# Kernel tuning notes

Measured on AMD Instinct MI355X. Metric: run time of the kernel, lower is better.

## Reference

```python
import jax, jax.numpy as jnp
import numpy as np

NUM_NODES = 200000
B = 65536          # n_id batch size
E = 131072         # events per direction
D_MEM = 128
D_RAW = 128
D_TIME = 128
T_MAX = 1000000


def setup_inputs() -> dict:
    key = jax.random.key(0)
    ks = jax.random.split(key, 16)
    inp = {
        'memory': jax.random.normal(ks[0], (NUM_NODES, D_MEM), jnp.float32),
        'last_update': jax.random.randint(ks[1], (NUM_NODES,), 0, 1000, jnp.int64),
        'n_id': jnp.arange(B, dtype=jnp.int64),
        'src_s': jax.random.randint(ks[2], (E,), 0, B, jnp.int64),
        'dst_s': jax.random.randint(ks[3], (E,), 0, B, jnp.int64),
        't_s': jax.random.randint(ks[4], (E,), 0, T_MAX, jnp.int64),
        'raw_msg_s': jax.random.normal(ks[5], (E, D_RAW), jnp.float32),
        'src_d': jax.random.randint(ks[6], (E,), 0, B, jnp.int64),
        'dst_d': jax.random.randint(ks[7], (E,), 0, B, jnp.int64),
        't_d': jax.random.randint(ks[8], (E,), 0, T_MAX, jnp.int64),
        'raw_msg_d': jax.random.normal(ks[9], (E, D_RAW), jnp.float32),
        'w_time': jax.random.normal(ks[10], (D_TIME, 1), jnp.float32) * 0.1,
        'b_time': jax.random.normal(ks[11], (D_TIME,), jnp.float32) * 0.1,
        'W_ih': jax.random.normal(ks[12], (3 * D_MEM, 2 * D_MEM + D_RAW + D_TIME), jnp.float32) * 0.05,
        'W_hh': jax.random.normal(ks[13], (3 * D_MEM, D_MEM), jnp.float32) * 0.05,
        'b_ih': jax.random.normal(ks[14], (3 * D_MEM,), jnp.float32) * 0.05,
        'b_hh': jax.random.normal(ks[15], (3 * D_MEM,), jnp.float32) * 0.05,
    }
    return inp


def _time_enc(t_rel, w_time, b_time):
    # Linear(1, time_dim) followed by cos: cos(t * w + b)
    return jnp.cos(t_rel.astype(jnp.float32)[:, None] * w_time[:, 0][None, :] + b_time)


def reference(memory, last_update, n_id, src_s, dst_s, t_s, raw_msg_s,
              src_d, dst_d, t_d, raw_msg_d, w_time, b_time, W_ih, W_hh, b_ih, b_hh):
    nb = n_id.shape[0]
    # assoc: global node id -> local index within n_id
    assoc = jnp.zeros((memory.shape[0],), dtype=jnp.int32).at[n_id].set(
        jnp.arange(nb, dtype=jnp.int32))

    # source-side messages (IdentityMessage = concat)
    t_enc_s = _time_enc(t_s - last_update[src_s], w_time, b_time)
    msg_s = jnp.concatenate([memory[src_s], memory[dst_s], raw_msg_s, t_enc_s], axis=-1)

    # destination-side messages
    t_enc_d = _time_enc(t_d - last_update[dst_d], w_time, b_time)
    msg_d = jnp.concatenate([memory[dst_d], memory[src_d], raw_msg_d, t_enc_d], axis=-1)

    idx = jnp.concatenate([src_s, dst_d], axis=0)       # [2E] global ids
    msg = jnp.concatenate([msg_s, msg_d], axis=0)       # [2E, 512]
    t = jnp.concatenate([t_s, t_d], axis=0)             # [2E]
    loc = assoc[idx]                                     # [2E] local ids

    # LastAggregator: per local node, pick the message with max t (ties -> latest position)
    ne = t.shape[0]
    key = t * ne + jnp.arange(ne, dtype=t.dtype)         # encode (t, position)
    maxkey = jax.ops.segment_max(key, loc, num_segments=nb)
    count = jax.ops.segment_sum(jnp.ones_like(loc), loc, num_segments=nb)
    has = count > 0
    argm = jnp.where(has, maxkey % ne, 0)
    aggr = jnp.where(has[:, None], msg[argm], 0.0)       # [nb, 512]

    # GRUCell(x=aggr, h=memory[n_id])
    h = memory[n_id]
    gi = aggr @ W_ih.T + b_ih
    gh = h @ W_hh.T + b_hh
    gi_r, gi_z, gi_n = jnp.split(gi, 3, axis=-1)
    gh_r, gh_z, gh_n = jnp.split(gh, 3, axis=-1)
    r = jax.nn.sigmoid(gi_r + gh_r)
    z = jax.nn.sigmoid(gi_z + gh_z)
    n = jnp.tanh(gi_n + r * gh_n)
    new_memory = (1.0 - z) * n + z * h

    new_last_update = last_update.at[idx].set(t)[n_id]
    return new_memory, new_last_update
```

## Files before the change

kernel.cpp:

```cpp
#include <hip/hip_runtime.h>
#include <math.h>

#define NB        65536
#define EV        131072
#define NE        (2*EV)
#define DM        128
#define NO2       512
#define BM        64
#define NST       10
#define THREADS   512

typedef float f32x4  __attribute__((ext_vector_type(4)));
typedef float f32x16 __attribute__((ext_vector_type(16)));
typedef int   i32x4  __attribute__((ext_vector_type(4)));
typedef int   i32x8  __attribute__((ext_vector_type(8)));
typedef unsigned long long u64;

__device__ __forceinline__ float fcos_rev(float rev) {
    float r; asm("v_cos_f32 %0, %1" : "=v"(r) : "v"(rev)); return r;
}
__device__ __forceinline__ float fexp2(float x) {
    float r; asm("v_exp_f32 %0, %1" : "=v"(r) : "v"(x)); return r;
}
__device__ __forceinline__ float frcp(float x) {
    float r; asm("v_rcp_f32 %0, %1" : "=v"(r) : "v"(x)); return r;
}
__device__ __forceinline__ float fast_cos(float arg) {
    double rv = (double)arg * 0.15915494309189535;
    rv -= floor(rv);
    return fcos_rev((float)rv);
}
__device__ __forceinline__ float fsigmoid(float x) {
    x = fminf(fmaxf(x, -30.f), 30.f);
    float e = fexp2(-1.44269504088896f * x);
    return frcp(1.f + e);
}
__device__ __forceinline__ float ftanh_(float x) {
    x = fminf(fmaxf(x, -15.f), 15.f);
    float e = fexp2(-2.88539008177793f * x);
    return (1.f - e) * frcp(1.f + e);
}

#if defined(__has_builtin) && __has_builtin(__builtin_amdgcn_cvt_pk_fp8_f32)
__device__ __forceinline__ unsigned pack4_fp8(float f0, float f1, float f2, float f3) {
    int v = __builtin_amdgcn_cvt_pk_fp8_f32(f0, f1, 0, false);
    v = __builtin_amdgcn_cvt_pk_fp8_f32(f2, f3, v, true);
    return (unsigned)v;
}
#else
__device__ __forceinline__ unsigned enc1_fp8(float x) {
    unsigned u = __float_as_uint(x);
    unsigned s = (u >> 24) & 0x80u;
    float a = fabsf(x);
    if (!(a >= 0.001953125f)) return s;
    if (a > 448.f) a = 448.f;
    int e; float mf = frexpf(a, &e);
    int E = e + 6, mant;
    if (E <= 0) {
        mant = (int)(a * 512.f + 0.5f);
        if (mant > 7) return s | 0x08u;
        return s | (unsigned)mant;
    }
    mant = (int)((mf * 2.f - 1.f) * 8.f + 0.5f);
    if (mant == 8) { mant = 0; ++E; }
    if (E > 15) { E = 15; mant = 6; }
    if (E == 15 && mant == 7) mant = 6;
    return s | (unsigned)(E << 3) | (unsigned)mant;
}
__device__ __forceinline__ unsigned pack4_fp8(float f0, float f1, float f2, float f3) {
    return enc1_fp8(f0) | (enc1_fp8(f1) << 8) | (enc1_fp8(f2) << 16) | (enc1_fp8(f3) << 24);
}
#endif

__global__ void prep_k(const int* __restrict__ src_s, const int* __restrict__ t_s,
                       const int* __restrict__ dst_d, const int* __restrict__ t_d,
                       u64* __restrict__ keyarr, u64* __restrict__ lukey,
                       const float* __restrict__ W_ih, const float* __restrict__ W_hh,
                       const float* __restrict__ b_ih, const float* __restrict__ b_hh,
                       unsigned char* __restrict__ wp8, float* __restrict__ bp) {
    int bid = blockIdx.x;
    if (bid < NE / 256) {
        int e = bid * 256 + threadIdx.x;
        int g, t;
        if (e < EV) { g = src_s[e];      t = t_s[e]; }
        else        { g = dst_d[e - EV]; t = t_d[e - EV]; }
        u64 key = ((u64)(unsigned)t << 18) + (u64)(unsigned)e + 1ull;
        atomicMax(&keyarr[g], key);
        u64 lk = ((u64)(unsigned)(e + 1) << 20) | (u64)(unsigned)t;
        atomicMax(&lukey[g], lk);
        return;
    }
    int idx = (bid - NE / 256) * 256 + threadIdx.x;
    int col = idx / 80, g = idx - col * 80;
    int step = g >> 3, sl = g & 7;
    int ck = ((sl >> 1) ^ ((col >> 1) & 3));
    int k0 = step * 64 + ck * 16 + (sl & 1) * 8;
    int d = col >> 2, gate = col & 3;
    float f[8];
    #pragma unroll
    for (int j = 0; j < 8; ++j) {
        int c = k0 + j;
        float v = 0.f;
        if (c < 512) {
            int row = (gate == 0) ? d : (gate == 1) ? 128 + d : (gate == 2) ? 256 + d : -1;
            if (row >= 0) v = W_ih[(size_t)row * 512 + c];
        } else {
            int ch = c - 512;
            int row = (gate == 0) ? d : (gate == 1) ? 128 + d : (gate == 3) ? 256 + d : -1;
            if (row >= 0) v = W_hh[(size_t)row * 128 + ch];
        }
        f[j] = v * 16.f;
    }
    unsigned lo = pack4_fp8(f[0], f[1], f[2], f[3]);
    unsigned hi = pack4_fp8(f[4], f[5], f[6], f[7]);
    *(u64*)(wp8 + (size_t)step * 32768 + (size_t)col * 64 + (size_t)sl * 8)
        = (u64)lo | ((u64)hi << 32);
    if (g == 0) {
        float bv = (gate == 0) ? b_ih[d] + b_hh[d]
                 : (gate == 1) ? b_ih[128 + d] + b_hh[128 + d]
                 : (gate == 2) ? b_ih[256 + d] : b_hh[256 + d];
        bp[col] = bv;
    }
}

__global__ __launch_bounds__(THREADS, 4) void gemm_gru_k(
    const float* __restrict__ memory, const int* __restrict__ last_update,
    const int* __restrict__ src_s, const int* __restrict__ dst_s,
    const int* __restrict__ t_s, const float* __restrict__ raw_s,
    const int* __restrict__ src_d, const int* __restrict__ dst_d,
    const int* __restrict__ t_d, const float* __restrict__ raw_d,
    const float* __restrict__ w_time, const float* __restrict__ b_time,
    const unsigned char* __restrict__ wp8, const float* __restrict__ bp,
    const u64* __restrict__ keyarr, const u64* __restrict__ lukey,
    float* __restrict__ out_mem, float* __restrict__ out_lu)
{
    __shared__ __align__(16) char smem[74752];
    unsigned char* sA = (unsigned char*)smem;
    unsigned char* sB = (unsigned char*)(smem + 8192);
    float* sW = (float*)(smem + 73728);
    float* sBt= (float*)(smem + 74240);

    const int tid = threadIdx.x;
    const int m0  = blockIdx.x * BM;
    const int ln  = tid & 63, wn = tid >> 6;
    const int lg  = ln >> 5;

    if (tid < DM) { sW[tid] = w_time[tid]; sBt[tid] = b_time[tid]; }

    const int ar = tid >> 3, ac = tid & 7;
    const int m  = m0 + ar;
    const u64 kk = keyarr[m];
    const int rv = (kk != 0ull);
    int a_ = 0, b_ = 0, t_ = 0;
    const float* pR = raw_s;
    if (kk) {
        int e = (int)((kk - 1ull) & (u64)(NE - 1));
        if (e < EV) { a_ = src_s[e]; b_ = dst_s[e]; t_ = t_s[e]; pR = raw_s + (size_t)e * DM; }
        else { int e2 = e - EV; a_ = dst_d[e2]; b_ = src_d[e2]; t_ = t_d[e2]; pR = raw_d + (size_t)e2 * DM; }
    }
    const float rt = rv ? (float)(t_ - last_update[a_]) : 0.f;
    const float* pA = memory + (size_t)a_ * DM;
    const float* pB = memory + (size_t)b_ * DM;
    const float* pH = memory + (size_t)m  * DM;

    float4 pv0, pv1;
    auto PREF_A = [&](int step) {
        int seg = step >> 1;
        if (seg == 3) return;
        const float* base = (seg == 0) ? pA : (seg == 1) ? pB : (seg == 2) ? pR : pH;
        int off = ((step & 1) << 6) + (ac << 3);
        pv0 = *(const float4*)(base + off);
        pv1 = *(const float4*)(base + off + 4);
    };
    auto STAGE_B = [&](int step, int buf) {
        const unsigned char* src = wp8 + (size_t)step * 32768 + (size_t)tid * 16;
        unsigned char* dst = sB + (size_t)buf * 32768 + (size_t)tid * 16;
        #pragma unroll
        for (int i = 0; i < 4; ++i)
            __builtin_amdgcn_global_load_lds(
                (const __attribute__((address_space(1))) void*)(src + i * 8192),
                (__attribute__((address_space(3))) void*)(dst + i * 8192), 16, 0, 0);
    };
    auto WRITE_A = [&](int step, int buf) {
        int seg = step >> 1;
        float f0, f1, f2, f3, f4, f5, f6, f7;
        if (seg == 3) {
            int coff = ((step & 1) << 6) + (ac << 3);
            f0 = fast_cos(__fadd_rn(__fmul_rn(rt, sW[coff+0]), sBt[coff+0]));
            f1 = fast_cos(__fadd_rn(__fmul_rn(rt, sW[coff+1]), sBt[coff+1]));
            f2 = fast_cos(__fadd_rn(__fmul_rn(rt, sW[coff+2]), sBt[coff+2]));
            f3 = fast_cos(__fadd_rn(__fmul_rn(rt, sW[coff+3]), sBt[coff+3]));
            f4 = fast_cos(__fadd_rn(__fmul_rn(rt, sW[coff+4]), sBt[coff+4]));
            f5 = fast_cos(__fadd_rn(__fmul_rn(rt, sW[coff+5]), sBt[coff+5]));
            f6 = fast_cos(__fadd_rn(__fmul_rn(rt, sW[coff+6]), sBt[coff+6]));
            f7 = fast_cos(__fadd_rn(__fmul_rn(rt, sW[coff+7]), sBt[coff+7]));
        } else {
            f0 = pv0.x; f1 = pv0.y; f2 = pv0.z; f3 = pv0.w;
            f4 = pv1.x; f5 = pv1.y; f6 = pv1.z; f7 = pv1.w;
        }
        if (seg < 4 && !rv) { f0=f1=f2=f3=f4=f5=f6=f7 = 0.f; }
        unsigned lo = pack4_fp8(f0, f1, f2, f3);
        unsigned hi = pack4_fp8(f4, f5, f6, f7);
        u64 q = (u64)lo | ((u64)hi << 32);
        *(u64*)(sA + buf * 4096 + ar * 64
                + (((ac >> 1) ^ ((ar >> 1) & 3)) << 4) + ((ac & 1) << 3)) = q;
    };

    f32x16 acc[2][2];
    #pragma unroll
    for (int mf = 0; mf < 2; ++mf)
        #pragma unroll
        for (int nf = 0; nf < 2; ++nf)
            #pragma unroll
            for (int j = 0; j < 16; ++j) acc[mf][nf][j] = 0.f;

    PREF_A(0);
    WRITE_A(0, 0);
    STAGE_B(0, 0);
    PREF_A(1);
    asm volatile("s_waitcnt vmcnt(2) lgkmcnt(0)" ::: "memory");
    __builtin_amdgcn_sched_barrier(0);
    __builtin_amdgcn_s_barrier();

    #pragma unroll
    for (int k = 0; k < NST; ++k) {
        const int cur = k & 1, nxt = cur ^ 1;

        if (k < NST - 1) {
            WRITE_A(k + 1, nxt);
            __builtin_amdgcn_sched_barrier(0);
            STAGE_B(k + 1, nxt);
            __builtin_amdgcn_sched_barrier(0);
        }

        i32x8 af[2], bf[2];
        #pragma unroll
        for (int mf = 0; mf < 2; ++mf) {
            int r = mf * 32 + (ln & 31), sw = (r >> 1) & 3;
            i32x4 q0 = *(const i32x4*)(sA + cur * 4096 + r * 64 + (((2*lg+0) ^ sw) << 4));
            i32x4 q1 = *(const i32x4*)(sA + cur * 4096 + r * 64 + (((2*lg+1) ^ sw) << 4));
            af[mf] = (i32x8){q0.x,q0.y,q0.z,q0.w, q1.x,q1.y,q1.z,q1.w};
        }
        #pragma unroll
        for (int nf = 0; nf < 2; ++nf) {
            int c = wn * 64 + nf * 32 + (ln & 31), sw = (c >> 1) & 3;
            i32x4 q0 = *(const i32x4*)(sB + cur * 32768 + c * 64 + (((2*lg+0) ^ sw) << 4));
            i32x4 q1 = *(const i32x4*)(sB + cur * 32768 + c * 64 + (((2*lg+1) ^ sw) << 4));
            bf[nf] = (i32x8){q0.x,q0.y,q0.z,q0.w, q1.x,q1.y,q1.z,q1.w};
        }
        __builtin_amdgcn_sched_barrier(0);

        const bool pf = (k + 2 <= NST - 1) && (((k + 2) >> 1) != 3);
        if (pf) PREF_A(k + 2);
        __builtin_amdgcn_sched_barrier(0);

        __builtin_amdgcn_s_setprio(1);
        #pragma unroll
        for (int mf = 0; mf < 2; ++mf)
            #pragma unroll
            for (int nf = 0; nf < 2; ++nf)
                acc[mf][nf] = __builtin_amdgcn_mfma_scale_f32_32x32x64_f8f6f4(
                    af[mf], bf[nf], acc[mf][nf], 0, 0, 0, 127, 0, 127);
        __builtin_amdgcn_s_setprio(0);

        if (k < NST - 1) {
            __builtin_amdgcn_sched_barrier(0);
            if (pf) asm volatile("s_waitcnt vmcnt(2) lgkmcnt(0)" ::: "memory");
            else    asm volatile("s_waitcnt vmcnt(0) lgkmcnt(0)" ::: "memory");
            __builtin_amdgcn_sched_barrier(0);
            __builtin_amdgcn_s_barrier();
        }
    }

    if (tid < BM) {
        u64 lk = lukey[m0 + tid];
        out_lu[m0 + tid] = lk ? (float)(unsigned)(lk & 0xFFFFFull)
                              : (float)last_update[m0 + tid];
    }
    __syncthreads();

    float* ep = (float*)(smem + wn * 8704);
    const int erow = ln >> 1, half = ln & 1;
    const int d0 = wn * 16 + half * 8;
    const float ds = 0.0625f;

    #pragma unroll
    for (int mf = 0; mf < 2; ++mf) {
        #pragma unroll
        for (int nf = 0; nf < 2; ++nf)
            #pragma unroll
            for (int reg = 0; reg < 16; ++reg) {
                int r32 = (reg & 3) + 8 * (reg >> 2) + 4 * lg;
                ep[r32 * 68 + nf * 32 + (ln & 31)] = acc[mf][nf][reg] * ds;
            }
        asm volatile("s_waitcnt lgkmcnt(0)" ::: "memory");

        const int gm = m0 + mf * 32 + erow;
        const float* gr = ep + erow * 68 + half * 32;
        float res[8];
        f32x4 h0 = *(const f32x4*)(memory + (size_t)gm * DM + d0);
        f32x4 h1 = *(const f32x4*)(memory + (size_t)gm * DM + d0 + 4);
        #pragma unroll
        for (int q = 0; q < 8; ++q) {
            f32x4 g  = *(const f32x4*)(gr + q * 4);
            f32x4 bb = *(const f32x4*)(bp + (d0 + q) * 4);
            float rg = fsigmoid(g.x + bb.x);
            float zg = fsigmoid(g.y + bb.y);
            float ng = ftanh_(g.z + bb.z + rg * (g.w + bb.w));
            float hh = (q < 4) ? ((const float*)&h0)[q] : ((const float*)&h1)[q - 4];
            res[q] = (1.f - zg) * ng + zg * hh;
        }
        *(f32x4*)(out_mem + (size_t)gm * DM + d0)     = *(const f32x4*)res;
        *(f32x4*)(out_mem + (size_t)gm * DM + d0 + 4) = *(const f32x4*)(res + 4);
        if (mf == 0) asm volatile("s_waitcnt lgkmcnt(0)" ::: "memory");
    }
}

extern "C" void kernel_launch(void* const* d_in, const int* in_sizes, int n_in,
                              void* d_out, int out_size, void* d_ws, size_t ws_size,
                              hipStream_t stream) {
    const float* memory      = (const float*)d_in[0];
    const int*   last_update = (const int*)d_in[1];
    const int*   src_s       = (const int*)d_in[3];
    const int*   dst_s       = (const int*)d_in[4];
    const int*   t_s         = (const int*)d_in[5];
    const float* raw_s       = (const float*)d_in[6];
    const int*   src_d       = (const int*)d_in[7];
    const int*   dst_d       = (const int*)d_in[8];
    const int*   t_d         = (const int*)d_in[9];
    const float* raw_d       = (const float*)d_in[10];
    const float* w_time      = (const float*)d_in[11];
    const float* b_time      = (const float*)d_in[12];
    const float* W_ih        = (const float*)d_in[13];
    const float* W_hh        = (const float*)d_in[14];
    const float* b_ih        = (const float*)d_in[15];
    const float* b_hh        = (const float*)d_in[16];

    char* ws = (char*)d_ws;
    u64* keyarr = (u64*)ws;
    u64* lukey  = (u64*)(ws + 524288);
    unsigned char* wp8 = (unsigned char*)(ws + 1048576);
    float* bp = (float*)(ws + 1376256);

    hipMemsetAsync(d_ws, 0, 1048576, stream);

    prep_k<<<NE / 256 + (NO2 * 80) / 256, 256, 0, stream>>>(
        src_s, t_s, dst_d, t_d, keyarr, lukey, W_ih, W_hh, b_ih, b_hh, wp8, bp);

    float* out_mem = (float*)d_out;
    float* out_lu  = out_mem + (size_t)NB * DM;
    gemm_gru_k<<<NB / BM, THREADS, 0, stream>>>(memory, last_update,
        src_s, dst_s, t_s, raw_s, src_d, dst_d, t_d, raw_d,
        w_time, b_time, wp8, bp, keyarr, lukey, out_mem, out_lu);
}
```

Before: 78.63 us.

## Enlarge GEMM tile to 128 rows with triple-buffered 16x16x32 FP8 MFMA pipeline

Doubles the row tile per block from 64 to 128 and splits the 8 waves into a 2x4 grid, each computing a 64x128 output sub-tile with 16x16x32 FP8 MFMAs in place of the scaled 32x32x64 instruction. A/B staging moves from double to triple buffering with a two-step lookahead, and the weight packing layout in prep changes to match. The goal is more reuse of each weight tile per block and better overlap of loads with MFMA work, at the cost of more LDS per block (occupancy cut to 2 blocks per CU), more barriers per step, and scalar instead of vector stores in the epilogue.

```diff
diff --git a/kernel.cpp b/kernel.cpp
--- a/kernel.cpp
+++ b/kernel.cpp
@@ -1,19 +1,16 @@
 #include <hip/hip_runtime.h>
 #include <math.h>
 
-#define NB        65536
-#define EV        131072
-#define NE        (2*EV)
-#define DM        128
-#define NO2       512
-#define BM        64
-#define NST       10
-#define THREADS   512
-
-typedef float f32x4  __attribute__((ext_vector_type(4)));
-typedef float f32x16 __attribute__((ext_vector_type(16)));
-typedef int   i32x4  __attribute__((ext_vector_type(4)));
-typedef int   i32x8  __attribute__((ext_vector_type(8)));
+#define NB 65536
+#define EV 131072
+#define NE (2*EV)
+#define DM 128
+#define BM 128
+#define NT 10
+#define THREADS 512
+
+typedef float f32x4 __attribute__((ext_vector_type(4)));
+typedef int   i32x4 __attribute__((ext_vector_type(4)));
 typedef unsigned long long u64;
 
 __device__ __forceinline__ float fcos_rev(float rev) {
@@ -91,10 +88,10 @@
         return;
     }
     int idx = (bid - NE / 256) * 256 + threadIdx.x;
-    int col = idx / 80, g = idx - col * 80;
-    int step = g >> 3, sl = g & 7;
-    int ck = ((sl >> 1) ^ ((col >> 1) & 3));
-    int k0 = step * 64 + ck * 16 + (sl & 1) * 8;
+    int t = idx >> 12, r = idx & 4095;
+    int col = r >> 3, slot = r & 7;
+    int g = slot ^ ((col >> 1) & 3);
+    int k0 = t * 64 + g * 8;
     int d = col >> 2, gate = col & 3;
     float f[8];
     #pragma unroll
@@ -113,9 +110,8 @@
     }
     unsigned lo = pack4_fp8(f[0], f[1], f[2], f[3]);
     unsigned hi = pack4_fp8(f[4], f[5], f[6], f[7]);
-    *(u64*)(wp8 + (size_t)step * 32768 + (size_t)col * 64 + (size_t)sl * 8)
-        = (u64)lo | ((u64)hi << 32);
-    if (g == 0) {
+    *(u64*)(wp8 + (size_t)idx * 8) = (u64)lo | ((u64)hi << 32);
+    if (k0 == 0) {
         float bv = (gate == 0) ? b_ih[d] + b_hh[d]
                  : (gate == 1) ? b_ih[128 + d] + b_hh[128 + d]
                  : (gate == 2) ? b_ih[256 + d] : b_hh[256 + d];
@@ -123,7 +119,7 @@
     }
 }
 
-__global__ __launch_bounds__(THREADS, 4) void gemm_gru_k(
+__global__ __launch_bounds__(THREADS, 2) void gemm_gru_k(
     const float* __restrict__ memory, const int* __restrict__ last_update,
     const int* __restrict__ src_s, const int* __restrict__ dst_s,
     const int* __restrict__ t_s, const float* __restrict__ raw_s,
@@ -134,20 +130,21 @@
     const u64* __restrict__ keyarr, const u64* __restrict__ lukey,
     float* __restrict__ out_mem, float* __restrict__ out_lu)
 {
-    __shared__ __align__(16) char smem[74752];
+    __shared__ __align__(16) char smem[123904];
     unsigned char* sA = (unsigned char*)smem;
-    unsigned char* sB = (unsigned char*)(smem + 8192);
-    float* sW = (float*)(smem + 73728);
-    float* sBt= (float*)(smem + 74240);
+    unsigned char* sB = (unsigned char*)(smem + 24576);
+    float* sW  = (float*)(smem + 122880);
+    float* sBt = (float*)(smem + 123392);
 
     const int tid = threadIdx.x;
     const int m0  = blockIdx.x * BM;
-    const int ln  = tid & 63, wn = tid >> 6;
-    const int lg  = ln >> 5;
+    const int ln  = tid & 63, wid = tid >> 6;
+    const int wr  = wid >> 2, wc = wid & 3;
+    const int l2  = ln >> 4, rl = ln & 15;
 
     if (tid < DM) { sW[tid] = w_time[tid]; sBt[tid] = b_time[tid]; }
 
-    const int ar = tid >> 3, ac = tid & 7;
+    const int ar = tid >> 2, kc = tid & 3;
     const int m  = m0 + ar;
     const u64 kk = keyarr[m];
     const int rv = (kk != 0ull);
@@ -163,112 +160,132 @@
     const float* pB = memory + (size_t)b_ * DM;
     const float* pH = memory + (size_t)m  * DM;
 
-    float4 pv0, pv1;
-    auto PREF_A = [&](int step) {
-        int seg = step >> 1;
-        if (seg == 3) return;
-        const float* base = (seg == 0) ? pA : (seg == 1) ? pB : (seg == 2) ? pR : pH;
-        int off = ((step & 1) << 6) + (ac << 3);
-        pv0 = *(const float4*)(base + off);
-        pv1 = *(const float4*)(base + off + 4);
+    float4 pv[4];
+    auto PREF_A = [&](int t) {
+        const float* base; int off;
+        if (t < 2)      { base = pA; off = (t & 1) * 64; }
+        else if (t < 4) { base = pB; off = (t & 1) * 64; }
+        else if (t < 6) { base = pR; off = (t & 1) * 64; }
+        else            { base = pH; off = (t - 8) * 64; }
+        const float* p = base + off + kc * 16;
+        pv[0] = *(const float4*)(p);
+        pv[1] = *(const float4*)(p + 4);
+        pv[2] = *(const float4*)(p + 8);
+        pv[3] = *(const float4*)(p + 12);
     };
-    auto STAGE_B = [&](int step, int buf) {
-        const unsigned char* src = wp8 + (size_t)step * 32768 + (size_t)tid * 16;
-        unsigned char* dst = sB + (size_t)buf * 32768 + (size_t)tid * 16;
+    auto GLL_B = [&](int t) {
+        const unsigned char* src = wp8 + (size_t)t * 32768 + (size_t)tid * 16;
+        unsigned char* dst = sB + (size_t)(t % 3) * 32768 + (size_t)tid * 16;
         #pragma unroll
         for (int i = 0; i < 4; ++i)
             __builtin_amdgcn_global_load_lds(
                 (const __attribute__((address_space(1))) void*)(src + i * 8192),
                 (__attribute__((address_space(3))) void*)(dst + i * 8192), 16, 0, 0);
     };
-    auto WRITE_A = [&](int step, int buf) {
-        int seg = step >> 1;
-        float f0, f1, f2, f3, f4, f5, f6, f7;
-        if (seg == 3) {
-            int coff = ((step & 1) << 6) + (ac << 3);
-            f0 = fast_cos(__fadd_rn(__fmul_rn(rt, sW[coff+0]), sBt[coff+0]));
-            f1 = fast_cos(__fadd_rn(__fmul_rn(rt, sW[coff+1]), sBt[coff+1]));
-            f2 = fast_cos(__fadd_rn(__fmul_rn(rt, sW[coff+2]), sBt[coff+2]));
-            f3 = fast_cos(__fadd_rn(__fmul_rn(rt, sW[coff+3]), sBt[coff+3]));
-            f4 = fast_cos(__fadd_rn(__fmul_rn(rt, sW[coff+4]), sBt[coff+4]));
-            f5 = fast_cos(__fadd_rn(__fmul_rn(rt, sW[coff+5]), sBt[coff+5]));
-            f6 = fast_cos(__fadd_rn(__fmul_rn(rt, sW[coff+6]), sBt[coff+6]));
-            f7 = fast_cos(__fadd_rn(__fmul_rn(rt, sW[coff+7]), sBt[coff+7]));
+    auto WRITE_A = [&](int t) {
+        unsigned p0, p1, p2, p3;
+        if (t >= 6 && t < 8) {
+            int coff = (t & 1) * 64 + kc * 16;
+            float c[16];
+            #pragma unroll
+            for (int j = 0; j < 16; ++j)
+                c[j] = fast_cos(__fadd_rn(__fmul_rn(rt, sW[coff + j]), sBt[coff + j]));
+            p0 = pack4_fp8(c[0], c[1], c[2], c[3]);
+            p1 = pack4_fp8(c[4], c[5], c[6], c[7]);
+            p2 = pack4_fp8(c[8], c[9], c[10], c[11]);
+            p3 = pack4_fp8(c[12], c[13], c[14], c[15]);
         } else {
-            f0 = pv0.x; f1 = pv0.y; f2 = pv0.z; f3 = pv0.w;
-            f4 = pv1.x; f5 = pv1.y; f6 = pv1.z; f7 = pv1.w;
+            p0 = pack4_fp8(pv[0].x, pv[0].y, pv[0].z, pv[0].w);
+            p1 = pack4_fp8(pv[1].x, pv[1].y, pv[1].z, pv[1].w);
+            p2 = pack4_fp8(pv[2].x, pv[2].y, pv[2].z, pv[2].w);
+            p3 = pack4_fp8(pv[3].x, pv[3].y, pv[3].z, pv[3].w);
         }
-        if (seg < 4 && !rv) { f0=f1=f2=f3=f4=f5=f6=f7 = 0.f; }
-        unsigned lo = pack4_fp8(f0, f1, f2, f3);
-        unsigned hi = pack4_fp8(f4, f5, f6, f7);
-        u64 q = (u64)lo | ((u64)hi << 32);
-        *(u64*)(sA + buf * 4096 + ar * 64
-                + (((ac >> 1) ^ ((ar >> 1) & 3)) << 4) + ((ac & 1) << 3)) = q;
+        if (t < 8 && !rv) { p0 = p1 = p2 = p3 = 0u; }
+        int swz = (ar >> 1) & 3;
+        i32x4 v = (swz & 1) ? (i32x4){(int)p2, (int)p3, (int)p0, (int)p1}
+                            : (i32x4){(int)p0, (int)p1, (int)p2, (int)p3};
+        *(i32x4*)(sA + (size_t)(t % 3) * 8192 + ar * 64 + (((2 * kc) ^ (swz & 2)) << 3)) = v;
     };
 
-    f32x16 acc[2][2];
+    f32x4 acc[4][8];
     #pragma unroll
-    for (int mf = 0; mf < 2; ++mf)
-        #pragma unroll
-        for (int nf = 0; nf < 2; ++nf)
-            #pragma unroll
-            for (int j = 0; j < 16; ++j) acc[mf][nf][j] = 0.f;
+    for (int mf = 0; mf < 4; ++mf)
+        #pragma unroll
+        for (int nf = 0; nf < 8; ++nf)
+            acc[mf][nf] = (f32x4){0.f, 0.f, 0.f, 0.f};
 
     PREF_A(0);
-    WRITE_A(0, 0);
-    STAGE_B(0, 0);
+    WRITE_A(0);
     PREF_A(1);
-    asm volatile("s_waitcnt vmcnt(2) lgkmcnt(0)" ::: "memory");
+    WRITE_A(1);
+    GLL_B(0);
+    GLL_B(1);
+    PREF_A(2);
+    asm volatile("s_waitcnt vmcnt(8) lgkmcnt(0)" ::: "memory");
     __builtin_amdgcn_sched_barrier(0);
     __builtin_amdgcn_s_barrier();
 
     #pragma unroll
-    for (int k = 0; k < NST; ++k) {
-        const int cur = k & 1, nxt = cur ^ 1;
-
-        if (k < NST - 1) {
-            WRITE_A(k + 1, nxt);
-            __builtin_amdgcn_sched_barrier(0);
-            STAGE_B(k + 1, nxt);
-            __builtin_amdgcn_sched_barrier(0);
-        }
-
-        i32x8 af[2], bf[2];
-        #pragma unroll
-        for (int mf = 0; mf < 2; ++mf) {
-            int r = mf * 32 + (ln & 31), sw = (r >> 1) & 3;
-            i32x4 q0 = *(const i32x4*)(sA + cur * 4096 + r * 64 + (((2*lg+0) ^ sw) << 4));
-            i32x4 q1 = *(const i32x4*)(sA + cur * 4096 + r * 64 + (((2*lg+1) ^ sw) << 4));
-            af[mf] = (i32x8){q0.x,q0.y,q0.z,q0.w, q1.x,q1.y,q1.z,q1.w};
-        }
-        #pragma unroll
-        for (int nf = 0; nf < 2; ++nf) {
-            int c = wn * 64 + nf * 32 + (ln & 31), sw = (c >> 1) & 3;
-            i32x4 q0 = *(const i32x4*)(sB + cur * 32768 + c * 64 + (((2*lg+0) ^ sw) << 4));
-            i32x4 q1 = *(const i32x4*)(sB + cur * 32768 + c * 64 + (((2*lg+1) ^ sw) << 4));
-            bf[nf] = (i32x8){q0.x,q0.y,q0.z,q0.w, q1.x,q1.y,q1.z,q1.w};
-        }
-        __builtin_amdgcn_sched_barrier(0);
-
-        const bool pf = (k + 2 <= NST - 1) && (((k + 2) >> 1) != 3);
-        if (pf) PREF_A(k + 2);
-        __builtin_amdgcn_sched_barrier(0);
-
-        __builtin_amdgcn_s_setprio(1);
-        #pragma unroll
-        for (int mf = 0; mf < 2; ++mf)
-            #pragma unroll
-            for (int nf = 0; nf < 2; ++nf)
-                acc[mf][nf] = __builtin_amdgcn_mfma_scale_f32_32x32x64_f8f6f4(
-                    af[mf], bf[nf], acc[mf][nf], 0, 0, 0, 127, 0, 127);
-        __builtin_amdgcn_s_setprio(0);
-
-        if (k < NST - 1) {
-            __builtin_amdgcn_sched_barrier(0);
-            if (pf) asm volatile("s_waitcnt vmcnt(2) lgkmcnt(0)" ::: "memory");
-            else    asm volatile("s_waitcnt vmcnt(0) lgkmcnt(0)" ::: "memory");
+    for (int t = 0; t < NT; ++t) {
+        #pragma unroll
+        for (int ph = 0; ph < 4; ++ph) {
+            const int mh = ph >> 1, nh = ph & 1;
+
+            long afr[2][2], bfr[4][2];
+            {
+                const unsigned char* aB = sA + (size_t)(t % 3) * 8192;
+                #pragma unroll
+                for (int mi = 0; mi < 2; ++mi) {
+                    int r = wr * 64 + (mh * 2 + mi) * 16 + rl;
+                    int so = ((l2 ^ ((r >> 1) & 3)) << 3);
+                    afr[mi][0] = *(const long*)(aB + r * 64 + so);
+                    afr[mi][1] = *(const long*)(aB + r * 64 + so + 32);
+                }
+                const unsigned char* bB = sB + (size_t)(t % 3) * 32768;
+                #pragma unroll
+                for (int ni = 0; ni < 4; ++ni) {
+                    int c = wc * 128 + (nh * 4 + ni) * 16 + rl;
+                    int so = ((l2 ^ ((c >> 1) & 3)) << 3);
+                    bfr[ni][0] = *(const long*)(bB + c * 64 + so);
+                    bfr[ni][1] = *(const long*)(bB + c * 64 + so + 32);
+                }
+            }
+            if (ph == 0 && t + 2 < NT) { WRITE_A(t + 2); GLL_B(t + 2); }
+            if (ph == 1 && t + 3 < NT && !(t + 3 == 6 || t + 3 == 7)) PREF_A(t + 3);
+
             __builtin_amdgcn_sched_barrier(0);
             __builtin_amdgcn_s_barrier();
+            asm volatile("s_waitcnt lgkmcnt(0)" ::: "memory");
+            __builtin_amdgcn_sched_barrier(0);
+
+            __builtin_amdgcn_s_setprio(1);
+            #pragma unroll
+            for (int ks = 0; ks < 2; ++ks)
+                #pragma unroll
+                for (int mi = 0; mi < 2; ++mi)
+                    #pragma unroll
+                    for (int ni = 0; ni < 4; ++ni)
+                        acc[mh * 2 + mi][nh * 4 + ni] =
+                            __builtin_amdgcn_mfma_f32_16x16x32_fp8_fp8(
+                                afr[mi][ks], bfr[ni][ks],
+                                acc[mh * 2 + mi][nh * 4 + ni], 0, 0, 0);
+            __builtin_amdgcn_s_setprio(0);
+            __builtin_amdgcn_sched_barrier(0);
+
+            if (ph == 3) {
+                if (t < NT - 1) {
+                    if (t == 3 || t == 4 || t == 7)
+                        asm volatile("s_waitcnt vmcnt(4) lgkmcnt(0)" ::: "memory");
+                    else if (t == 8)
+                        asm volatile("s_waitcnt vmcnt(0) lgkmcnt(0)" ::: "memory");
+                    else
+                        asm volatile("s_waitcnt vmcnt(8) lgkmcnt(0)" ::: "memory");
+                    __builtin_amdgcn_sched_barrier(0);
+                    __builtin_amdgcn_s_barrier();
+                }
+            } else {
+                __builtin_amdgcn_s_barrier();
+            }
         }
     }
 
@@ -279,40 +296,33 @@
     }
     __syncthreads();
 
-    float* ep = (float*)(smem + wn * 8704);
-    const int erow = ln >> 1, half = ln & 1;
-    const int d0 = wn * 16 + half * 8;
-    const float ds = 0.0625f;
+    float* ep = (float*)(smem + wid * 8448);
+    const int row16 = ln >> 2, dq = ln & 3;
+    const int d8 = wc * 32 + dq * 8;
+    const float dsc = 0.0625f;
 
     #pragma unroll
-    for (int mf = 0; mf < 2; ++mf) {
-        #pragma unroll
-        for (int nf = 0; nf < 2; ++nf)
+    for (int mf = 0; mf < 4; ++mf) {
+        #pragma unroll
+        for (int nf = 0; nf < 8; ++nf)
             #pragma unroll
-            for (int reg = 0; reg < 16; ++reg) {
-                int r32 = (reg & 3) + 8 * (reg >> 2) + 4 * lg;
-                ep[r32 * 68 + nf * 32 + (ln & 31)] = acc[mf][nf][reg] * ds;
-            }
+            for (int reg = 0; reg < 4; ++reg)
+                ep[(l2 * 4 + reg) * 132 + nf * 16 + rl] = acc[mf][nf][reg] * dsc;
         asm volatile("s_waitcnt lgkmcnt(0)" ::: "memory");
 
-        const int gm = m0 + mf * 32 + erow;
-        const float* gr = ep + erow * 68 + half * 32;
-        float res[8];
-        f32x4 h0 = *(const f32x4*)(memory + (size_t)gm * DM + d0);
-        f32x4 h1 = *(const f32x4*)(memory + (size_t)gm * DM + d0 + 4);
+        const int gm = m0 + wr * 64 + mf * 16 + row16;
         #pragma unroll
         for (int q = 0; q < 8; ++q) {
-            f32x4 g  = *(const f32x4*)(gr + q * 4);
-            f32x4 bb = *(const f32x4*)(bp + (d0 + q) * 4);
+            int q2 = (q + dq) & 7;
+            f32x4 g  = *(const f32x4*)(ep + row16 * 132 + dq * 32 + q2 * 4);
+            f32x4 bb = *(const f32x4*)(bp + (size_t)(d8 + q2) * 4);
             float rg = fsigmoid(g.x + bb.x);
             float zg = fsigmoid(g.y + bb.y);
             float ng = ftanh_(g.z + bb.z + rg * (g.w + bb.w));
-            float hh = (q < 4) ? ((const float*)&h0)[q] : ((const float*)&h1)[q - 4];
-            res[q] = (1.f - zg) * ng + zg * hh;
+            float hh = memory[(size_t)gm * DM + d8 + q2];
+            out_mem[(size_t)gm * DM + d8 + q2] = (1.f - zg) * ng + zg * hh;
         }
-        *(f32x4*)(out_mem + (size_t)gm * DM + d0)     = *(const f32x4*)res;
-        *(f32x4*)(out_mem + (size_t)gm * DM + d0 + 4) = *(const f32x4*)(res + 4);
-        if (mf == 0) asm volatile("s_waitcnt lgkmcnt(0)" ::: "memory");
+        if (mf < 3) asm volatile("s_waitcnt lgkmcnt(0)" ::: "memory");
     }
 }
 
@@ -344,7 +354,7 @@
 
     hipMemsetAsync(d_ws, 0, 1048576, stream);
 
-    prep_k<<<NE / 256 + (NO2 * 80) / 256, 256, 0, stream>>>(
+    prep_k<<<NE / 256 + 160, 256, 0, stream>>>(
         src_s, t_s, dst_d, t_d, keyarr, lukey, W_ih, W_hh, b_ih, b_hh, wp8, bp);
 
     float* out_mem = (float*)d_out;
```

Measured after the change: 109.6 us. 39.4% more time.

## Split activation gather and fp8 packing into a separate kernel before the GEMM

Applied to the files above, without the earlier changes.

The gather of memory rows, raw messages and the time-encoding cosines moves out of the GEMM main loop into a new build kernel. That kernel writes a pre-swizzled fp8 A matrix into the output buffer, which is reused as scratch. The GEMM kernel then streams A tiles straight into LDS with async loads, just as it does for B, and only packs the hidden-state rows itself. The weight-packing layout is rewritten to 16-byte chunks. The aim is to take irregular gathers and transcendental work off the MFMA critical path, at the cost of an extra launch and an extra global write and read of the packed A matrix.

```diff
diff --git a/kernel.cpp b/kernel.cpp
--- a/kernel.cpp
+++ b/kernel.cpp
@@ -1,14 +1,13 @@
 #include <hip/hip_runtime.h>
 #include <math.h>
 
-#define NB        65536
-#define EV        131072
-#define NE        (2*EV)
-#define DM        128
-#define NO2       512
-#define BM        64
-#define NST       10
-#define THREADS   512
+#define NB 65536
+#define EV 131072
+#define NE (2*EV)
+#define DM 128
+#define BM 64
+#define NT 10
+#define THREADS 512
 
 typedef float f32x4  __attribute__((ext_vector_type(4)));
 typedef float f32x16 __attribute__((ext_vector_type(16)));
@@ -72,85 +71,73 @@
 }
 #endif
 
-__global__ void prep_k(const int* __restrict__ src_s, const int* __restrict__ t_s,
+__global__ void scan_k(const int* __restrict__ src_s, const int* __restrict__ t_s,
                        const int* __restrict__ dst_d, const int* __restrict__ t_d,
-                       u64* __restrict__ keyarr, u64* __restrict__ lukey,
-                       const float* __restrict__ W_ih, const float* __restrict__ W_hh,
-                       const float* __restrict__ b_ih, const float* __restrict__ b_hh,
-                       unsigned char* __restrict__ wp8, float* __restrict__ bp) {
+                       u64* __restrict__ keyarr, u64* __restrict__ lukey) {
+    int e = blockIdx.x * 256 + threadIdx.x;
+    int g, t;
+    if (e < EV) { g = src_s[e];      t = t_s[e]; }
+    else        { g = dst_d[e - EV]; t = t_d[e - EV]; }
+    u64 key = ((u64)(unsigned)t << 18) + (u64)(unsigned)e + 1ull;
+    atomicMax(&keyarr[g], key);
+    u64 lk = ((u64)(unsigned)(e + 1) << 20) | (u64)(unsigned)t;
+    atomicMax(&lukey[g], lk);
+}
+
+__global__ void build_k(const u64* __restrict__ keyarr, const u64* __restrict__ lukey,
+                        const float* __restrict__ memory, const int* __restrict__ last_update,
+                        const int* __restrict__ src_s, const int* __restrict__ dst_s,
+                        const int* __restrict__ t_s, const float* __restrict__ raw_s,
+                        const int* __restrict__ src_d, const int* __restrict__ dst_d,
+                        const int* __restrict__ t_d, const float* __restrict__ raw_d,
+                        const float* __restrict__ w_time, const float* __restrict__ b_time,
+                        const float* __restrict__ W_ih, const float* __restrict__ W_hh,
+                        const float* __restrict__ b_ih, const float* __restrict__ b_hh,
+                        unsigned char* __restrict__ wp8, float* __restrict__ bp,
+                        unsigned char* __restrict__ a8, float* __restrict__ out_lu) {
     int bid = blockIdx.x;
-    if (bid < NE / 256) {
-        int e = bid * 256 + threadIdx.x;
-        int g, t;
-        if (e < EV) { g = src_s[e];      t = t_s[e]; }
-        else        { g = dst_d[e - EV]; t = t_d[e - EV]; }
-        u64 key = ((u64)(unsigned)t << 18) + (u64)(unsigned)e + 1ull;
-        atomicMax(&keyarr[g], key);
-        u64 lk = ((u64)(unsigned)(e + 1) << 20) | (u64)(unsigned)t;
-        atomicMax(&lukey[g], lk);
+    if (bid < 80) {
+        int idx = bid * 256 + threadIdx.x;
+        int t = idx >> 11, r = idx & 2047;
+        int c = r >> 2, pg = r & 3;
+        int g = pg ^ ((c >> 1) & 3);
+        int k0 = t * 64 + g * 16;
+        int d = c >> 2, gate = c & 3;
+        float f[16];
+        #pragma unroll
+        for (int j = 0; j < 16; ++j) {
+            int k = k0 + j;
+            float v = 0.f;
+            if (k < 512) {
+                int row = (gate == 0) ? d : (gate == 1) ? 128 + d : (gate == 2) ? 256 + d : -1;
+                if (row >= 0) v = W_ih[(size_t)row * 512 + k];
+            } else {
+                int ch = k - 512;
+                int row = (gate == 0) ? d : (gate == 1) ? 128 + d : (gate == 3) ? 256 + d : -1;
+                if (row >= 0) v = W_hh[(size_t)row * 128 + ch];
+            }
+            f[j] = v * 16.f;
+        }
+        i32x4 v;
+        v.x = (int)pack4_fp8(f[0], f[1], f[2], f[3]);
+        v.y = (int)pack4_fp8(f[4], f[5], f[6], f[7]);
+        v.z = (int)pack4_fp8(f[8], f[9], f[10], f[11]);
+        v.w = (int)pack4_fp8(f[12], f[13], f[14], f[15]);
+        *(i32x4*)(wp8 + (size_t)idx * 16) = v;
+        if (k0 == 0) {
+            float bv = (gate == 0) ? b_ih[d] + b_hh[d]
+                     : (gate == 1) ? b_ih[128 + d] + b_hh[128 + d]
+                     : (gate == 2) ? b_ih[256 + d] : b_hh[256 + d];
+            bp[c] = bv;
+        }
         return;
     }
-    int idx = (bid - NE / 256) * 256 + threadIdx.x;
-    int col = idx / 80, g = idx - col * 80;
-    int step = g >> 3, sl = g & 7;
-    int ck = ((sl >> 1) ^ ((col >> 1) & 3));
-    int k0 = step * 64 + ck * 16 + (sl & 1) * 8;
-    int d = col >> 2, gate = col & 3;
-    float f[8];
-    #pragma unroll
-    for (int j = 0; j < 8; ++j) {
-        int c = k0 + j;
-        float v = 0.f;
-        if (c < 512) {
-            int row = (gate == 0) ? d : (gate == 1) ? 128 + d : (gate == 2) ? 256 + d : -1;
-            if (row >= 0) v = W_ih[(size_t)row * 512 + c];
-        } else {
-            int ch = c - 512;
-            int row = (gate == 0) ? d : (gate == 1) ? 128 + d : (gate == 3) ? 256 + d : -1;
-            if (row >= 0) v = W_hh[(size_t)row * 128 + ch];
-        }
-        f[j] = v * 16.f;
-    }
-    unsigned lo = pack4_fp8(f[0], f[1], f[2], f[3]);
-    unsigned hi = pack4_fp8(f[4], f[5], f[6], f[7]);
-    *(u64*)(wp8 + (size_t)step * 32768 + (size_t)col * 64 + (size_t)sl * 8)
-        = (u64)lo | ((u64)hi << 32);
-    if (g == 0) {
-        float bv = (gate == 0) ? b_ih[d] + b_hh[d]
-                 : (gate == 1) ? b_ih[128 + d] + b_hh[128 + d]
-                 : (gate == 2) ? b_ih[256 + d] : b_hh[256 + d];
-        bp[col] = bv;
-    }
-}
-
-__global__ __launch_bounds__(THREADS, 4) void gemm_gru_k(
-    const float* __restrict__ memory, const int* __restrict__ last_update,
-    const int* __restrict__ src_s, const int* __restrict__ dst_s,
-    const int* __restrict__ t_s, const float* __restrict__ raw_s,
-    const int* __restrict__ src_d, const int* __restrict__ dst_d,
-    const int* __restrict__ t_d, const float* __restrict__ raw_d,
-    const float* __restrict__ w_time, const float* __restrict__ b_time,
-    const unsigned char* __restrict__ wp8, const float* __restrict__ bp,
-    const u64* __restrict__ keyarr, const u64* __restrict__ lukey,
-    float* __restrict__ out_mem, float* __restrict__ out_lu)
-{
-    __shared__ __align__(16) char smem[74752];
-    unsigned char* sA = (unsigned char*)smem;
-    unsigned char* sB = (unsigned char*)(smem + 8192);
-    float* sW = (float*)(smem + 73728);
-    float* sBt= (float*)(smem + 74240);
-
-    const int tid = threadIdx.x;
-    const int m0  = blockIdx.x * BM;
-    const int ln  = tid & 63, wn = tid >> 6;
-    const int lg  = ln >> 5;
-
-    if (tid < DM) { sW[tid] = w_time[tid]; sBt[tid] = b_time[tid]; }
-
-    const int ar = tid >> 3, ac = tid & 7;
-    const int m  = m0 + ar;
-    const u64 kk = keyarr[m];
-    const int rv = (kk != 0ull);
+    int blk = bid - 80;
+    int m0 = blk * 64;
+    int r = threadIdx.x >> 2, pg = threadIdx.x & 3;
+    int m = m0 + r;
+    u64 kk = keyarr[m];
+    int rv = (kk != 0ull);
     int a_ = 0, b_ = 0, t_ = 0;
     const float* pR = raw_s;
     if (kk) {
@@ -161,19 +148,80 @@
     const float rt = rv ? (float)(t_ - last_update[a_]) : 0.f;
     const float* pA = memory + (size_t)a_ * DM;
     const float* pB = memory + (size_t)b_ * DM;
-    const float* pH = memory + (size_t)m  * DM;
-
-    float4 pv0, pv1;
-    auto PREF_A = [&](int step) {
-        int seg = step >> 1;
-        if (seg == 3) return;
-        const float* base = (seg == 0) ? pA : (seg == 1) ? pB : (seg == 2) ? pR : pH;
-        int off = ((step & 1) << 6) + (ac << 3);
-        pv0 = *(const float4*)(base + off);
-        pv1 = *(const float4*)(base + off + 4);
+    if (pg == 0) {
+        u64 lk = lukey[m];
+        out_lu[m] = lk ? (float)(unsigned)(lk & 0xFFFFFull) : (float)last_update[m];
+    }
+    const int g = pg ^ ((r >> 1) & 3);
+    unsigned char* dst = a8 + (size_t)blk * 32768 + (size_t)threadIdx.x * 16;
+    #pragma unroll
+    for (int t = 0; t < 8; ++t) {
+        int koff = t * 64 + g * 16;
+        int seg = koff >> 7, off = koff & 127;
+        float f[16];
+        if (seg == 3) {
+            f32x4 w0 = *(const f32x4*)(w_time + off),     w1 = *(const f32x4*)(w_time + off + 4);
+            f32x4 w2 = *(const f32x4*)(w_time + off + 8), w3 = *(const f32x4*)(w_time + off + 12);
+            f32x4 c0 = *(const f32x4*)(b_time + off),     c1 = *(const f32x4*)(b_time + off + 4);
+            f32x4 c2 = *(const f32x4*)(b_time + off + 8), c3 = *(const f32x4*)(b_time + off + 12);
+            const float* wv = (const float*)&w0; const float* cv = (const float*)&c0;
+            float wa[16] = {w0.x,w0.y,w0.z,w0.w,w1.x,w1.y,w1.z,w1.w,w2.x,w2.y,w2.z,w2.w,w3.x,w3.y,w3.z,w3.w};
+            float ca[16] = {c0.x,c0.y,c0.z,c0.w,c1.x,c1.y,c1.z,c1.w,c2.x,c2.y,c2.z,c2.w,c3.x,c3.y,c3.z,c3.w};
+            (void)wv; (void)cv;
+            #pragma unroll
+            for (int j = 0; j < 16; ++j)
+                f[j] = fast_cos(__fadd_rn(__fmul_rn(rt, wa[j]), ca[j]));
+        } else {
+            const float* base = (seg == 0) ? pA : (seg == 1) ? pB : pR;
+            f32x4 q0 = *(const f32x4*)(base + off);
+            f32x4 q1 = *(const f32x4*)(base + off + 4);
+            f32x4 q2 = *(const f32x4*)(base + off + 8);
+            f32x4 q3 = *(const f32x4*)(base + off + 12);
+            f[0]=q0.x; f[1]=q0.y; f[2]=q0.z; f[3]=q0.w;
+            f[4]=q1.x; f[5]=q1.y; f[6]=q1.z; f[7]=q1.w;
+            f[8]=q2.x; f[9]=q2.y; f[10]=q2.z; f[11]=q2.w;
+            f[12]=q3.x; f[13]=q3.y; f[14]=q3.z; f[15]=q3.w;
+        }
+        if (!rv) {
+            #pragma unroll
+            for (int j = 0; j < 16; ++j) f[j] = 0.f;
+        }
+        i32x4 v;
+        v.x = (int)pack4_fp8(f[0], f[1], f[2], f[3]);
+        v.y = (int)pack4_fp8(f[4], f[5], f[6], f[7]);
+        v.z = (int)pack4_fp8(f[8], f[9], f[10], f[11]);
+        v.w = (int)pack4_fp8(f[12], f[13], f[14], f[15]);
+        *(i32x4*)(dst + t * 4096) = v;
+    }
+}
+
+__global__ __launch_bounds__(THREADS, 4) void gemm_k(
+    const float* __restrict__ memory,
+    const unsigned char* __restrict__ a8,
+    const unsigned char* __restrict__ wp8,
+    const float* __restrict__ bp,
+    float* __restrict__ out_mem)
+{
+    __shared__ __align__(16) char smem[73728];
+    unsigned char* sA = (unsigned char*)smem;
+    unsigned char* sB = (unsigned char*)(smem + 8192);
+
+    const int tid = threadIdx.x;
+    const int m0  = blockIdx.x * BM;
+    const int ln  = tid & 63, wn = tid >> 6;
+    const int lg  = ln >> 5;
+
+    auto STAGE_A = [&](int t, int buf) {
+        if (tid < 256) {
+            const unsigned char* src = a8 + (size_t)blockIdx.x * 32768
+                                          + (size_t)t * 4096 + (size_t)tid * 16;
+            __builtin_amdgcn_global_load_lds(
+                (const __attribute__((address_space(1))) void*)src,
+                (__attribute__((address_space(3))) void*)(sA + buf * 4096 + tid * 16), 16, 0, 0);
+        }
     };
-    auto STAGE_B = [&](int step, int buf) {
-        const unsigned char* src = wp8 + (size_t)step * 32768 + (size_t)tid * 16;
+    auto STAGE_B = [&](int t, int buf) {
+        const unsigned char* src = wp8 + (size_t)t * 32768 + (size_t)tid * 16;
         unsigned char* dst = sB + (size_t)buf * 32768 + (size_t)tid * 16;
         #pragma unroll
         for (int i = 0; i < 4; ++i)
@@ -181,29 +229,22 @@
                 (const __attribute__((address_space(1))) void*)(src + i * 8192),
                 (__attribute__((address_space(3))) void*)(dst + i * 8192), 16, 0, 0);
     };
-    auto WRITE_A = [&](int step, int buf) {
-        int seg = step >> 1;
-        float f0, f1, f2, f3, f4, f5, f6, f7;
-        if (seg == 3) {
-            int coff = ((step & 1) << 6) + (ac << 3);
-            f0 = fast_cos(__fadd_rn(__fmul_rn(rt, sW[coff+0]), sBt[coff+0]));
-            f1 = fast_cos(__fadd_rn(__fmul_rn(rt, sW[coff+1]), sBt[coff+1]));
-            f2 = fast_cos(__fadd_rn(__fmul_rn(rt, sW[coff+2]), sBt[coff+2]));
-            f3 = fast_cos(__fadd_rn(__fmul_rn(rt, sW[coff+3]), sBt[coff+3]));
-            f4 = fast_cos(__fadd_rn(__fmul_rn(rt, sW[coff+4]), sBt[coff+4]));
-            f5 = fast_cos(__fadd_rn(__fmul_rn(rt, sW[coff+5]), sBt[coff+5]));
-            f6 = fast_cos(__fadd_rn(__fmul_rn(rt, sW[coff+6]), sBt[coff+6]));
-            f7 = fast_cos(__fadd_rn(__fmul_rn(rt, sW[coff+7]), sBt[coff+7]));
-        } else {
-            f0 = pv0.x; f1 = pv0.y; f2 = pv0.z; f3 = pv0.w;
-            f4 = pv1.x; f5 = pv1.y; f6 = pv1.z; f7 = pv1.w;
-        }
-        if (seg < 4 && !rv) { f0=f1=f2=f3=f4=f5=f6=f7 = 0.f; }
-        unsigned lo = pack4_fp8(f0, f1, f2, f3);
-        unsigned hi = pack4_fp8(f4, f5, f6, f7);
-        u64 q = (u64)lo | ((u64)hi << 32);
-        *(u64*)(sA + buf * 4096 + ar * 64
-                + (((ac >> 1) ^ ((ar >> 1) & 3)) << 4) + ((ac & 1) << 3)) = q;
+    auto STAGE_H = [&](int t, int buf) {
+        if (tid < 256) {
+            int r = tid >> 2, pg = tid & 3;
+            int g = pg ^ ((r >> 1) & 3);
+            const float* hp = memory + (size_t)(m0 + r) * DM + (t - 8) * 64 + g * 16;
+            f32x4 q0 = *(const f32x4*)(hp);
+            f32x4 q1 = *(const f32x4*)(hp + 4);
+            f32x4 q2 = *(const f32x4*)(hp + 8);
+            f32x4 q3 = *(const f32x4*)(hp + 12);
+            i32x4 v;
+            v.x = (int)pack4_fp8(q0.x, q0.y, q0.z, q0.w);
+            v.y = (int)pack4_fp8(q1.x, q1.y, q1.z, q1.w);
+            v.z = (int)pack4_fp8(q2.x, q2.y, q2.z, q2.w);
+            v.w = (int)pack4_fp8(q3.x, q3.y, q3.z, q3.w);
+            *(i32x4*)(sA + buf * 4096 + tid * 16) = v;
+        }
     };
 
     f32x16 acc[2][2];
@@ -214,24 +255,21 @@
             #pragma unroll
             for (int j = 0; j < 16; ++j) acc[mf][nf][j] = 0.f;
 
-    PREF_A(0);
-    WRITE_A(0, 0);
+    STAGE_A(0, 0);
     STAGE_B(0, 0);
-    PREF_A(1);
-    asm volatile("s_waitcnt vmcnt(2) lgkmcnt(0)" ::: "memory");
+    asm volatile("s_waitcnt vmcnt(0) lgkmcnt(0)" ::: "memory");
     __builtin_amdgcn_sched_barrier(0);
     __builtin_amdgcn_s_barrier();
 
     #pragma unroll
-    for (int k = 0; k < NST; ++k) {
+    for (int k = 0; k < NT; ++k) {
         const int cur = k & 1, nxt = cur ^ 1;
 
-        if (k < NST - 1) {
-            WRITE_A(k + 1, nxt);
-            __builtin_amdgcn_sched_barrier(0);
+        if (k < NT - 1) {
+            if (k + 1 < 8) STAGE_A(k + 1, nxt); else STAGE_H(k + 1, nxt);
             STAGE_B(k + 1, nxt);
-            __builtin_amdgcn_sched_barrier(0);
-        }
+        }
+        __builtin_amdgcn_sched_barrier(0);
 
         i32x8 af[2], bf[2];
         #pragma unroll
@@ -248,10 +286,7 @@
             i32x4 q1 = *(const i32x4*)(sB + cur * 32768 + c * 64 + (((2*lg+1) ^ sw) << 4));
             bf[nf] = (i32x8){q0.x,q0.y,q0.z,q0.w, q1.x,q1.y,q1.z,q1.w};
         }
-        __builtin_amdgcn_sched_barrier(0);
-
-        const bool pf = (k + 2 <= NST - 1) && (((k + 2) >> 1) != 3);
-        if (pf) PREF_A(k + 2);
+        asm volatile("s_waitcnt lgkmcnt(0)" ::: "memory");
         __builtin_amdgcn_sched_barrier(0);
 
         __builtin_amdgcn_s_setprio(1);
@@ -263,20 +298,14 @@
                     af[mf], bf[nf], acc[mf][nf], 0, 0, 0, 127, 0, 127);
         __builtin_amdgcn_s_setprio(0);
 
-        if (k < NST - 1) {
+        if (k < NT - 1) {
             __builtin_amdgcn_sched_barrier(0);
-            if (pf) asm volatile("s_waitcnt vmcnt(2) lgkmcnt(0)" ::: "memory");
-            else    asm volatile("s_waitcnt vmcnt(0) lgkmcnt(0)" ::: "memory");
+            asm volatile("s_waitcnt vmcnt(0) lgkmcnt(0)" ::: "memory");
             __builtin_amdgcn_sched_barrier(0);
             __builtin_amdgcn_s_barrier();
         }
     }
 
-    if (tid < BM) {
-        u64 lk = lukey[m0 + tid];
-        out_lu[m0 + tid] = lk ? (float)(unsigned)(lk & 0xFFFFFull)
-                              : (float)last_update[m0 + tid];
-    }
     __syncthreads();
 
     float* ep = (float*)(smem + wn * 8704);
@@ -342,14 +371,15 @@
     unsigned char* wp8 = (unsigned char*)(ws + 1048576);
     float* bp = (float*)(ws + 1376256);
 
-    hipMemsetAsync(d_ws, 0, 1048576, stream);
-
-    prep_k<<<NE / 256 + (NO2 * 80) / 256, 256, 0, stream>>>(
-        src_s, t_s, dst_d, t_d, keyarr, lukey, W_ih, W_hh, b_ih, b_hh, wp8, bp);
-
     float* out_mem = (float*)d_out;
     float* out_lu  = out_mem + (size_t)NB * DM;
-    gemm_gru_k<<<NB / BM, THREADS, 0, stream>>>(memory, last_update,
+    unsigned char* a8 = (unsigned char*)d_out;
+
+    hipMemsetAsync(d_ws, 0, 1048576, stream);
+
+    scan_k<<<NE / 256, 256, 0, stream>>>(src_s, t_s, dst_d, t_d, keyarr, lukey);
+    build_k<<<80 + NB / 64, 256, 0, stream>>>(keyarr, lukey, memory, last_update,
         src_s, dst_s, t_s, raw_s, src_d, dst_d, t_d, raw_d,
-        w_time, b_time, wp8, bp, keyarr, lukey, out_mem, out_lu);
-}
+        w_time, b_time, W_ih, W_hh, b_ih, b_hh, wp8, bp, a8, out_lu);
+    gemm_k<<<NB / BM, THREADS, 0, stream>>>(memory, a8, wp8, bp, out_mem);
+}
```

Result: slower. 93.02 us (+18.3%).
